# Kernel tuning notes

Measured on AMD Instinct MI355X. Metric: run time of the kernel, lower is better.

Reference implementation:

```python
import jax, jax.numpy as jnp
import numpy as np

N_NODES = 100000
N_EDGES = 1600000
IN_FEAT, HIDDEN, N_CLASSES = 512, 32, 16


def setup_inputs() -> dict:
    key = jax.random.key(0)
    k1, k2, k3, k4 = jax.random.split(key, 4)
    x = jax.random.normal(k1, (N_NODES, IN_FEAT), dtype=jnp.float32)
    edge_index = jax.random.randint(k2, (2, N_EDGES), 0, N_NODES, dtype=jnp.int64)
    W1 = jax.random.normal(k3, (IN_FEAT, HIDDEN), dtype=jnp.float32) * (1.0 / np.sqrt(IN_FEAT))
    b1 = jnp.zeros((HIDDEN,), dtype=jnp.float32)
    W2 = jax.random.normal(k4, (HIDDEN, N_CLASSES), dtype=jnp.float32) * (1.0 / np.sqrt(HIDDEN))
    b2 = jnp.zeros((N_CLASSES,), dtype=jnp.float32)
    return {"x": x, "edge_index": edge_index, "W1": W1, "b1": b1, "W2": W2, "b2": b2}


def gcn_conv(x, row, col, norm, W, b, n_nodes):
    # linear transform first (PyG GCNConv order), then gather-scale-scatter
    h = x @ W                                   # [N, F_out]
    msg = h[row] * norm[:, None]                # edge-gather + normalize
    out = jax.ops.segment_sum(msg, col, num_segments=n_nodes)
    return out + b


def gcn_norm(edge_index, n_nodes):
    # add self-loops, symmetric normalization deg^{-1/2}[row]*deg^{-1/2}[col]
    loop = jnp.arange(n_nodes, dtype=edge_index.dtype)
    row = jnp.concatenate([edge_index[0], loop])
    col = jnp.concatenate([edge_index[1], loop])
    deg = jax.ops.segment_sum(jnp.ones_like(col, dtype=jnp.float32), col, num_segments=n_nodes)
    dis = jnp.where(deg > 0, jax.lax.rsqrt(jnp.maximum(deg, 1.0)), 0.0)
    norm = dis[row] * dis[col]
    return row, col, norm


def reference(x, edge_index, W1, b1, W2, b2):
    n_nodes = x.shape[0]
    row, col, norm = gcn_norm(edge_index, n_nodes)
    h = gcn_conv(x, row, col, norm, W1, b1, n_nodes)
    h = jax.nn.relu(h)
    # dropout p=0.5 in eval mode -> identity (deterministic baseline)
    h = gcn_conv(h, row, col, norm, W2, b2, n_nodes)
    return jax.nn.log_softmax(h, axis=1)
```

## Files before the change

kernel.cpp:

```cpp
#include <hip/hip_runtime.h>
#include <hip/hip_bf16.h>

#define NN 100000
#define NE 1600000
#define FIN 512
#define FH 32
#define FC 16
#define NCB2 ((NE / 8 + 255) / 256)
#define M_SL 32
#define SLICE (NE / M_SL)
#define QSL (SLICE / 4)
#define PSZ 32768
#define NP ((NN + PSZ - 1) / PSZ)
#define NHB (M_SL * NP)
#define NGB1 ((NN + 63) / 64)
#define XW (NN / 4)
#define XSB ((XW + 255) / 256)
#define SOS_NB 98
#define SCALE_B ((NN * 8 + 1023) / 1024)

typedef __attribute__((ext_vector_type(8))) short bf16x8;
typedef __attribute__((ext_vector_type(4))) float f32x4;

__device__ inline unsigned short f2bf(float f) {
    unsigned u = __float_as_uint(f);
    return (unsigned short)((u + 0x7FFFu + ((u >> 16) & 1u)) >> 16);
}
__device__ inline float bf2f(unsigned short u) {
    return __uint_as_float(((unsigned)u) << 16);
}
__device__ inline unsigned pk2bf(float a, float b) {
    __hip_bfloat162 p = __float22bfloat162_rn(make_float2(a, b));
    union { __hip_bfloat162 h; unsigned u; } c;
    c.h = p;
    return c.u;
}


__global__ __launch_bounds__(256) void k_prep(const float* __restrict__ W1,
                                              unsigned short* __restrict__ wbuf) {
    for (int idx = threadIdx.x; idx < 16 * 2 * 64; idx += 256) {
        int s = idx >> 7;
        int t = (idx >> 6) & 1;
        int l = idx & 63;
        int k0 = s * 32 + (l >> 4) * 8;
        int c = t * 16 + (l & 15);
        bf16x8 w;
#pragma unroll
        for (int i = 0; i < 8; ++i) w[i] = (short)f2bf(W1[(size_t)(k0 + i) * FH + c]);
        *(bf16x8*)(wbuf + (size_t)idx * 8) = w;
    }
}


__global__ __launch_bounds__(256) void k_hist_gemm1(const int* __restrict__ col,
                                                    unsigned char* __restrict__ ghist,
                                                    unsigned char* __restrict__ rank,
                                                    const float* __restrict__ x,
                                                    const unsigned short* __restrict__ wbuf,
                                                    unsigned* __restrict__ h1p) {
    __shared__ int sh[PSZ / 4];

    if (blockIdx.x >= NGB1) {
        int hb = blockIdx.x - NGB1;
        int p = hb / M_SL;
        int m = hb % M_SL;
        int base = p * PSZ;
        int nb = min(PSZ, NN - base);
        int nw = (nb + 3) >> 2;
        unsigned* shw = (unsigned*)sh;
        for (int i = threadIdx.x; i < nw; i += 256) shw[i] = 0u;
        __syncthreads();
        const int4* c4p = (const int4*)(col + m * SLICE);
        for (int it = 0; it < (QSL + 255) / 256; ++it) {
            int q = it * 256 + threadIdx.x;
            if (q < QSL) {
                int4 c4 = c4p[q];
                int e = m * SLICE + q * 4;
                int cc[4] = {c4.x, c4.y, c4.z, c4.w};
#pragma unroll
                for (int u = 0; u < 4; ++u) {
                    int d = cc[u] - base;
                    if ((unsigned)d < (unsigned)nb) {
                        int sft = 8 * (d & 3);
                        unsigned old = atomicAdd(&shw[d >> 2], 1u << sft);
                        rank[e + u] = (unsigned char)((old >> sft) & 0xFFu);
                    }
                }
            }
        }
        __syncthreads();
        unsigned* gdst = (unsigned*)(ghist + (size_t)m * NN + base);
        for (int i = threadIdx.x; i < nw; i += 256) gdst[i] = shw[i];
        return;
    }

    unsigned short* lb = (unsigned short*)sh;
    for (int i = threadIdx.x; i < 2048; i += 256)
        ((int4*)lb)[i] = ((const int4*)wbuf)[i];
    __syncthreads();

    int wave = threadIdx.x >> 6;
    int lane = threadIdx.x & 63;
    int rowbase = blockIdx.x * 64 + wave * 16;
    int arow = rowbase + (lane & 15);
    int arowc = min(arow, NN - 1);
    int kgrp = (lane >> 4) * 8;

    f32x4 acc0 = {0.f, 0.f, 0.f, 0.f};
    f32x4 acc1 = {0.f, 0.f, 0.f, 0.f};
    const float* xrow = x + (size_t)arowc * FIN + kgrp;

    for (int sg = 0; sg < 16; sg += 4) {
        float4 av[8];
#pragma unroll
        for (int u = 0; u < 4; ++u) {
            av[2 * u]     = *(const float4*)(xrow + (sg + u) * 32);
            av[2 * u + 1] = *(const float4*)(xrow + (sg + u) * 32 + 4);
        }
#pragma unroll
        for (int u = 0; u < 4; ++u) {
            const float* s0 = (const float*)&av[2 * u];
            const float* s1 = (const float*)&av[2 * u + 1];
            union { bf16x8 v; unsigned w[4]; } af;
            af.w[0] = pk2bf(s0[0], s0[1]);
            af.w[1] = pk2bf(s0[2], s0[3]);
            af.w[2] = pk2bf(s1[0], s1[1]);
            af.w[3] = pk2bf(s1[2], s1[3]);
            int s = sg + u;
            bf16x8 b0 = *(const bf16x8*)(lb + ((size_t)(s * 2 + 0) * 64 + lane) * 8);
            bf16x8 b1 = *(const bf16x8*)(lb + ((size_t)(s * 2 + 1) * 64 + lane) * 8);
            acc0 = __builtin_amdgcn_mfma_f32_16x16x32_bf16(af.v, b0, acc0, 0, 0, 0);
            acc1 = __builtin_amdgcn_mfma_f32_16x16x32_bf16(af.v, b1, acc1, 0, 0, 0);
        }
    }

    int crow = rowbase + (lane >> 4) * 4;
    int ccol = lane & 15;
#pragma unroll
    for (int r = 0; r < 4; ++r) {
        if (crow + r < NN)
            h1p[(size_t)(crow + r) * 16 + ccol] = pk2bf(acc0[r], acc1[r]);
    }
}


__global__ __launch_bounds__(256) void k_xscan(unsigned* __restrict__ ghistw,
                                               int* __restrict__ cnt,
                                               float* __restrict__ dis,
                                               int* __restrict__ part) {
    __shared__ int red[256];
    int widx = blockIdx.x * 256 + threadIdx.x;
    int tot = 0;
    if (widx < XW) {
        unsigned s0 = 0, s1 = 0, s2 = 0, s3 = 0;
        unsigned* p = ghistw + widx;
#pragma unroll 4
        for (int m = 0; m < M_SL; ++m) {
            unsigned w = p[(size_t)m * XW];
            p[(size_t)m * XW] = s0 | (s1 << 8) | (s2 << 16) | (s3 << 24);
            s0 += w & 0xFFu; s1 += (w >> 8) & 0xFFu;
            s2 += (w >> 16) & 0xFFu; s3 += (w >> 24) & 0xFFu;
        }
        int c0 = widx * 4;
        *(int4*)(cnt + c0) = make_int4(s0, s1, s2, s3);
        *(float4*)(dis + c0) = make_float4(rsqrtf((float)s0 + 1.f), rsqrtf((float)s1 + 1.f),
                                           rsqrtf((float)s2 + 1.f), rsqrtf((float)s3 + 1.f));
        tot = s0 + s1 + s2 + s3;
    }
    red[threadIdx.x] = tot;
    __syncthreads();
    for (int st = 128; st > 0; st >>= 1) {
        if (threadIdx.x < st) red[threadIdx.x] += red[threadIdx.x + st];
        __syncthreads();
    }
    if (threadIdx.x == 0) part[blockIdx.x] = red[0];
}


__global__ __launch_bounds__(1024) void k_scan_off_scale(const int* __restrict__ cnt,
                                                         const int* __restrict__ part,
                                                         int* __restrict__ off,
                                                         const uint2* __restrict__ h1p2,
                                                         uint2* __restrict__ h1s2,
                                                         const float* __restrict__ dis) {
    int bid = blockIdx.x;
    if (bid < SOS_NB) {
        __shared__ int s[1024];
        __shared__ int sp[128];
        if (threadIdx.x < 128) sp[threadIdx.x] = (threadIdx.x < XSB) ? part[threadIdx.x] : 0;
        __syncthreads();
        for (int st = 1; st < 128; st <<= 1) {
            int a = (threadIdx.x < 128 && threadIdx.x >= st) ? sp[threadIdx.x - st] : 0;
            __syncthreads();
            if (threadIdx.x < 128) sp[threadIdx.x] += a;
            __syncthreads();
        }
        int pbase = (bid == 0) ? 0 : sp[bid - 1];
        int i = bid * 1024 + threadIdx.x;
        int v = (i < NN) ? cnt[i] : 0;
        s[threadIdx.x] = v;
        __syncthreads();
        for (int st = 1; st < 1024; st <<= 1) {
            int a = (threadIdx.x >= st) ? s[threadIdx.x - st] : 0;
            __syncthreads();
            s[threadIdx.x] += a;
            __syncthreads();
        }
        if (i < NN) off[i] = pbase + s[threadIdx.x] - v;
        if (i == NN - 1) off[NN] = pbase + s[threadIdx.x];
    } else {
        int idx = (bid - SOS_NB) * 1024 + threadIdx.x;
        if (idx < NN * 8) {
            uint2 v = h1p2[idx];
            float d = dis[idx >> 3];
            float a0 = bf2f((unsigned short)v.x), a1 = bf2f((unsigned short)(v.x >> 16));
            float a2 = bf2f((unsigned short)v.y), a3 = bf2f((unsigned short)(v.y >> 16));
            uint2 o;
            o.x = pk2bf(a0 * d, a1 * d);
            o.y = pk2bf(a2 * d, a3 * d);
            h1s2[idx] = o;
        }
    }
}


__global__ void k_fill(const int* __restrict__ row, const int* __restrict__ col,
                       const unsigned char* __restrict__ rank,
                       const int* __restrict__ off,
                       const unsigned char* __restrict__ ghist,
                       int* __restrict__ esrc) {
    int t = blockIdx.x * blockDim.x + threadIdx.x;
    if (t >= NE / 8) return;
#pragma unroll
    for (int qq = 0; qq < 2; ++qq) {
        int i = t * 2 + qq;
        int m = i / QSL;
        int4 r4 = ((const int4*)row)[i];
        int4 c4 = ((const int4*)col)[i];
        uchar4 rk4 = ((const uchar4*)rank)[i];
        int rr[4] = {r4.x, r4.y, r4.z, r4.w};
        int cc[4] = {c4.x, c4.y, c4.z, c4.w};
        int rk[4] = {rk4.x, rk4.y, rk4.z, rk4.w};
        int o4[4], bp[4];
#pragma unroll
        for (int u = 0; u < 4; ++u) o4[u] = off[cc[u]];
#pragma unroll
        for (int u = 0; u < 4; ++u) bp[u] = ghist[(size_t)m * NN + cc[u]];
#pragma unroll
        for (int u = 0; u < 4; ++u) esrc[o4[u] + bp[u] + rk[u]] = rr[u];
    }
}


__global__ __launch_bounds__(256) void k_gather1g2(const int* __restrict__ off,
                                                   const int* __restrict__ esrc,
                                                   const unsigned* __restrict__ h1s,
                                                   const float* __restrict__ dis,
                                                   const float* __restrict__ b1,
                                                   const float* __restrict__ W2,
                                                   float* __restrict__ h2s) {
    __shared__ float w2l[FH * FC];
    __shared__ float hrl[32][FH + 2];
    for (int i = threadIdx.x; i < FH * FC; i += 256) w2l[i] = W2[i];

    int ng = threadIdx.x >> 3;
    int l = threadIdx.x & 7;
    int g = blockIdx.x * 32 + ng;
    int s0 = off[g], s1 = off[g + 1];
    const uint2* hp = (const uint2*)h1s + l;
    float a00 = 0.f, a01 = 0.f, a02 = 0.f, a03 = 0.f;
    float a10 = 0.f, a11 = 0.f, a12 = 0.f, a13 = 0.f;
    float a20 = 0.f, a21 = 0.f, a22 = 0.f, a23 = 0.f;
    float a30 = 0.f, a31 = 0.f, a32 = 0.f, a33 = 0.f;
    int i = s0;
    for (; i + 3 < s1; i += 4) {
        int r0 = esrc[i], r1 = esrc[i + 1], r2 = esrc[i + 2], r3 = esrc[i + 3];
        uint2 w0 = hp[(size_t)r0 * 8];
        uint2 w1 = hp[(size_t)r1 * 8];
        uint2 w2 = hp[(size_t)r2 * 8];
        uint2 w3 = hp[(size_t)r3 * 8];
        a00 += bf2f((unsigned short)w0.x); a01 += bf2f((unsigned short)(w0.x >> 16));
        a02 += bf2f((unsigned short)w0.y); a03 += bf2f((unsigned short)(w0.y >> 16));
        a10 += bf2f((unsigned short)w1.x); a11 += bf2f((unsigned short)(w1.x >> 16));
        a12 += bf2f((unsigned short)w1.y); a13 += bf2f((unsigned short)(w1.y >> 16));
        a20 += bf2f((unsigned short)w2.x); a21 += bf2f((unsigned short)(w2.x >> 16));
        a22 += bf2f((unsigned short)w2.y); a23 += bf2f((unsigned short)(w2.y >> 16));
        a30 += bf2f((unsigned short)w3.x); a31 += bf2f((unsigned short)(w3.x >> 16));
        a32 += bf2f((unsigned short)w3.y); a33 += bf2f((unsigned short)(w3.y >> 16));
    }
    for (; i < s1; ++i) {
        uint2 w = hp[(size_t)esrc[i] * 8];
        a00 += bf2f((unsigned short)w.x); a01 += bf2f((unsigned short)(w.x >> 16));
        a02 += bf2f((unsigned short)w.y); a03 += bf2f((unsigned short)(w.y >> 16));
    }
    uint2 ws = hp[(size_t)g * 8];
    float f0 = a00 + a10 + a20 + a30 + bf2f((unsigned short)ws.x);
    float f16 = a01 + a11 + a21 + a31 + bf2f((unsigned short)(ws.x >> 16));
    float f1 = a02 + a12 + a22 + a32 + bf2f((unsigned short)ws.y);
    float f17 = a03 + a13 + a23 + a33 + bf2f((unsigned short)(ws.y >> 16));
    float dg = dis[g];
    float2 blo = ((const float2*)b1)[l];
    float2 bhi = ((const float2*)b1)[l + 8];
    float v0 = dg * f0 + blo.x;
    float v1 = dg * f1 + blo.y;
    float v16 = dg * f16 + bhi.x;
    float v17 = dg * f17 + bhi.y;
    *(float2*)&hrl[ng][2 * l] = make_float2(v0 > 0.f ? v0 : 0.f, v1 > 0.f ? v1 : 0.f);
    *(float2*)&hrl[ng][2 * l + 16] = make_float2(v16 > 0.f ? v16 : 0.f, v17 > 0.f ? v17 : 0.f);
    __syncthreads();

    int j = threadIdx.x & 15;
#pragma unroll
    for (int half = 0; half < 2; ++half) {
        int n2 = (threadIdx.x >> 4) + half * 16;
        int g2 = blockIdx.x * 32 + n2;
        float s = 0.0f;
#pragma unroll
        for (int k = 0; k < FH; ++k) s += hrl[n2][k] * w2l[k * FC + j];
        h2s[(size_t)g2 * FC + j] = s * dis[g2];
    }
}


__global__ __launch_bounds__(256) void k_gather2(const int* __restrict__ off,
                                                 const int* __restrict__ esrc,
                                                 const float* __restrict__ h2s,
                                                 const float* __restrict__ dis,
                                                 const float* __restrict__ b2,
                                                 float* __restrict__ out) {
    int ng = threadIdx.x >> 2;
    int l = threadIdx.x & 3;
    int g = blockIdx.x * 64 + ng;
    if (g >= NN) return;
    int s0 = off[g], s1 = off[g + 1];
    const float4* hp = (const float4*)h2s + l;
    float ax0 = 0.f, ay0 = 0.f, az0 = 0.f, aw0 = 0.f;
    float ax1 = 0.f, ay1 = 0.f, az1 = 0.f, aw1 = 0.f;
    float ax2 = 0.f, ay2 = 0.f, az2 = 0.f, aw2 = 0.f;
    float ax3 = 0.f, ay3 = 0.f, az3 = 0.f, aw3 = 0.f;
    int i = s0;
    for (; i + 3 < s1; i += 4) {
        int r0 = esrc[i], r1 = esrc[i + 1], r2 = esrc[i + 2], r3 = esrc[i + 3];
        float4 t0 = hp[(size_t)r0 * 4];
        float4 t1 = hp[(size_t)r1 * 4];
        float4 t2 = hp[(size_t)r2 * 4];
        float4 t3 = hp[(size_t)r3 * 4];
        ax0 += t0.x; ay0 += t0.y; az0 += t0.z; aw0 += t0.w;
        ax1 += t1.x; ay1 += t1.y; az1 += t1.z; aw1 += t1.w;
        ax2 += t2.x; ay2 += t2.y; az2 += t2.z; aw2 += t2.w;
        ax3 += t3.x; ay3 += t3.y; az3 += t3.z; aw3 += t3.w;
    }
    for (; i < s1; ++i) {
        float4 t = hp[(size_t)esrc[i] * 4];
        ax0 += t.x; ay0 += t.y; az0 += t.z; aw0 += t.w;
    }
    float4 ts = hp[(size_t)g * 4];
    float vx = ax0 + ax1 + ax2 + ax3 + ts.x;
    float vy = ay0 + ay1 + ay2 + ay3 + ts.y;
    float vz = az0 + az1 + az2 + az3 + ts.z;
    float vw = aw0 + aw1 + aw2 + aw3 + ts.w;
    float dg = dis[g];
    float4 bb = ((const float4*)b2)[l];
    vx = dg * vx + bb.x;
    vy = dg * vy + bb.y;
    vz = dg * vz + bb.z;
    vw = dg * vw + bb.w;
    float m = fmaxf(fmaxf(vx, vy), fmaxf(vz, vw));
#pragma unroll
    for (int o = 1; o < 4; o <<= 1) m = fmaxf(m, __shfl_xor(m, o, 4));
    float e = __expf(vx - m) + __expf(vy - m) + __expf(vz - m) + __expf(vw - m);
    float s = e;
#pragma unroll
    for (int o = 1; o < 4; o <<= 1) s += __shfl_xor(s, o, 4);
    float ls = m + logf(s);
    ((float4*)out)[(size_t)g * 4 + l] = make_float4(vx - ls, vy - ls, vz - ls, vw - ls);
}

extern "C" void kernel_launch(void* const* d_in, const int* in_sizes, int n_in,
                              void* d_out, int out_size, void* d_ws, size_t ws_size,
                              hipStream_t stream) {
    const float* x  = (const float*)d_in[0];
    const int*   ei = (const int*)d_in[1];
    const float* W1 = (const float*)d_in[2];
    const float* b1 = (const float*)d_in[3];
    const float* W2 = (const float*)d_in[4];
    const float* b2 = (const float*)d_in[5];
    float* out = (float*)d_out;

    const int* row = ei;
    const int* col = ei + NE;

    int* base = (int*)d_ws;
    unsigned char* ghist = (unsigned char*)base;
    unsigned char* rank  = ghist + (size_t)M_SL * NN;
    int*   cnt   = base + 800000 + 400000;
    int*   off   = cnt + NN;
    int*   part  = off + NN + 8;
    float* dis   = (float*)(part + 128);
    unsigned short* wbuf = (unsigned short*)(dis + NN);
    unsigned* h1p = (unsigned*)(wbuf + 16384);
    unsigned* h1s = h1p + (size_t)NN * 16;
    int*   esrc  = (int*)(h1s + (size_t)NN * 16);
    float* h2s   = (float*)h1p;

    const int B = 256;

    k_prep<<<1, B, 0, stream>>>(W1, wbuf);
    k_hist_gemm1<<<NGB1 + NHB, B, 0, stream>>>(col, ghist, rank, x, wbuf, h1p);
    k_xscan<<<XSB, B, 0, stream>>>((unsigned*)ghist, cnt, dis, part);
    k_scan_off_scale<<<SOS_NB + SCALE_B, 1024, 0, stream>>>(cnt, part, off,
                                                            (const uint2*)h1p, (uint2*)h1s, dis);
    k_fill<<<NCB2, B, 0, stream>>>(row, col, rank, off, ghist, esrc);
    k_gather1g2<<<NN / 32, B, 0, stream>>>(off, esrc, h1s, dis, b1, W2, h2s);
    k_gather2<<<(NN + 63) / 64, B, 0, stream>>>(off, esrc, h2s, dis, b2, out);
}
```

Measured before the change: 168.1 us.

## Precompute per-slice bucket bases and widen gather1 to 16-byte row loads

The scan kernel now writes a combined per-slice base array (offset plus slice histogram) so the fill kernel does one random int load per edge instead of two random loads (off and ghist). Separately, the first gather kernel now uses 4 lanes per node with uint4 (8 bf16) loads and 64 nodes per block instead of 8 lanes with uint2 loads, halving the number of scattered load instructions per edge. This costs an extra 32*NN int array written in the scan kernel and more accumulator registers in gather1.

```diff
diff --git a/kernel.cpp b/kernel.cpp
--- a/kernel.cpp
+++ b/kernel.cpp
@@ -181,6 +181,8 @@
 __global__ __launch_bounds__(1024) void k_scan_off_scale(const int* __restrict__ cnt,
                                                          const int* __restrict__ part,
                                                          int* __restrict__ off,
+                                                         const unsigned char* __restrict__ ghist,
+                                                         int* __restrict__ cb,
                                                          const uint2* __restrict__ h1p2,
                                                          uint2* __restrict__ h1s2,
                                                          const float* __restrict__ dis) {
@@ -207,7 +209,13 @@
             s[threadIdx.x] += a;
             __syncthreads();
         }
-        if (i < NN) off[i] = pbase + s[threadIdx.x] - v;
+        if (i < NN) {
+            int o = pbase + s[threadIdx.x] - v;
+            off[i] = o;
+#pragma unroll 4
+            for (int m = 0; m < M_SL; ++m)
+                cb[(size_t)m * NN + i] = o + (int)ghist[(size_t)m * NN + i];
+        }
         if (i == NN - 1) off[NN] = pbase + s[threadIdx.x];
     } else {
         int idx = (bid - SOS_NB) * 1024 + threadIdx.x;
@@ -227,8 +235,7 @@
 
 __global__ void k_fill(const int* __restrict__ row, const int* __restrict__ col,
                        const unsigned char* __restrict__ rank,
-                       const int* __restrict__ off,
-                       const unsigned char* __restrict__ ghist,
+                       const int* __restrict__ cb,
                        int* __restrict__ esrc) {
     int t = blockIdx.x * blockDim.x + threadIdx.x;
     if (t >= NE / 8) return;
@@ -242,83 +249,106 @@
         int rr[4] = {r4.x, r4.y, r4.z, r4.w};
         int cc[4] = {c4.x, c4.y, c4.z, c4.w};
         int rk[4] = {rk4.x, rk4.y, rk4.z, rk4.w};
-        int o4[4], bp[4];
-#pragma unroll
-        for (int u = 0; u < 4; ++u) o4[u] = off[cc[u]];
-#pragma unroll
-        for (int u = 0; u < 4; ++u) bp[u] = ghist[(size_t)m * NN + cc[u]];
-#pragma unroll
-        for (int u = 0; u < 4; ++u) esrc[o4[u] + bp[u] + rk[u]] = rr[u];
+        int b4[4];
+#pragma unroll
+        for (int u = 0; u < 4; ++u) b4[u] = cb[(size_t)m * NN + cc[u]];
+#pragma unroll
+        for (int u = 0; u < 4; ++u) esrc[b4[u] + rk[u]] = rr[u];
     }
 }
 
 
 __global__ __launch_bounds__(256) void k_gather1g2(const int* __restrict__ off,
                                                    const int* __restrict__ esrc,
-                                                   const unsigned* __restrict__ h1s,
+                                                   const uint4* __restrict__ h1s4,
                                                    const float* __restrict__ dis,
                                                    const float* __restrict__ b1,
                                                    const float* __restrict__ W2,
                                                    float* __restrict__ h2s) {
     __shared__ float w2l[FH * FC];
-    __shared__ float hrl[32][FH + 2];
+    __shared__ float hrl[64][FH + 4];
     for (int i = threadIdx.x; i < FH * FC; i += 256) w2l[i] = W2[i];
 
-    int ng = threadIdx.x >> 3;
-    int l = threadIdx.x & 7;
-    int g = blockIdx.x * 32 + ng;
-    int s0 = off[g], s1 = off[g + 1];
-    const uint2* hp = (const uint2*)h1s + l;
-    float a00 = 0.f, a01 = 0.f, a02 = 0.f, a03 = 0.f;
-    float a10 = 0.f, a11 = 0.f, a12 = 0.f, a13 = 0.f;
-    float a20 = 0.f, a21 = 0.f, a22 = 0.f, a23 = 0.f;
-    float a30 = 0.f, a31 = 0.f, a32 = 0.f, a33 = 0.f;
-    int i = s0;
-    for (; i + 3 < s1; i += 4) {
-        int r0 = esrc[i], r1 = esrc[i + 1], r2 = esrc[i + 2], r3 = esrc[i + 3];
-        uint2 w0 = hp[(size_t)r0 * 8];
-        uint2 w1 = hp[(size_t)r1 * 8];
-        uint2 w2 = hp[(size_t)r2 * 8];
-        uint2 w3 = hp[(size_t)r3 * 8];
-        a00 += bf2f((unsigned short)w0.x); a01 += bf2f((unsigned short)(w0.x >> 16));
-        a02 += bf2f((unsigned short)w0.y); a03 += bf2f((unsigned short)(w0.y >> 16));
-        a10 += bf2f((unsigned short)w1.x); a11 += bf2f((unsigned short)(w1.x >> 16));
-        a12 += bf2f((unsigned short)w1.y); a13 += bf2f((unsigned short)(w1.y >> 16));
-        a20 += bf2f((unsigned short)w2.x); a21 += bf2f((unsigned short)(w2.x >> 16));
-        a22 += bf2f((unsigned short)w2.y); a23 += bf2f((unsigned short)(w2.y >> 16));
-        a30 += bf2f((unsigned short)w3.x); a31 += bf2f((unsigned short)(w3.x >> 16));
-        a32 += bf2f((unsigned short)w3.y); a33 += bf2f((unsigned short)(w3.y >> 16));
-    }
-    for (; i < s1; ++i) {
-        uint2 w = hp[(size_t)esrc[i] * 8];
-        a00 += bf2f((unsigned short)w.x); a01 += bf2f((unsigned short)(w.x >> 16));
-        a02 += bf2f((unsigned short)w.y); a03 += bf2f((unsigned short)(w.y >> 16));
-    }
-    uint2 ws = hp[(size_t)g * 8];
-    float f0 = a00 + a10 + a20 + a30 + bf2f((unsigned short)ws.x);
-    float f16 = a01 + a11 + a21 + a31 + bf2f((unsigned short)(ws.x >> 16));
-    float f1 = a02 + a12 + a22 + a32 + bf2f((unsigned short)ws.y);
-    float f17 = a03 + a13 + a23 + a33 + bf2f((unsigned short)(ws.y >> 16));
-    float dg = dis[g];
-    float2 blo = ((const float2*)b1)[l];
-    float2 bhi = ((const float2*)b1)[l + 8];
-    float v0 = dg * f0 + blo.x;
-    float v1 = dg * f1 + blo.y;
-    float v16 = dg * f16 + bhi.x;
-    float v17 = dg * f17 + bhi.y;
-    *(float2*)&hrl[ng][2 * l] = make_float2(v0 > 0.f ? v0 : 0.f, v1 > 0.f ? v1 : 0.f);
-    *(float2*)&hrl[ng][2 * l + 16] = make_float2(v16 > 0.f ? v16 : 0.f, v17 > 0.f ? v17 : 0.f);
+    int ng = threadIdx.x >> 2;
+    int l = threadIdx.x & 3;
+    int g = blockIdx.x * 64 + ng;
+    if (g < NN) {
+        int s0 = off[g], s1 = off[g + 1];
+        const uint4* hp = h1s4 + l;
+        float acc[4][8];
+#pragma unroll
+        for (int u = 0; u < 4; ++u)
+#pragma unroll
+            for (int k = 0; k < 8; ++k) acc[u][k] = 0.f;
+        int i = s0;
+        for (; i + 3 < s1; i += 4) {
+            int r0 = esrc[i], r1 = esrc[i + 1], r2 = esrc[i + 2], r3 = esrc[i + 3];
+            uint4 w0 = hp[(size_t)r0 * 4];
+            uint4 w1 = hp[(size_t)r1 * 4];
+            uint4 w2 = hp[(size_t)r2 * 4];
+            uint4 w3 = hp[(size_t)r3 * 4];
+            acc[0][0] += bf2f((unsigned short)w0.x); acc[0][1] += bf2f((unsigned short)(w0.x >> 16));
+            acc[0][2] += bf2f((unsigned short)w0.y); acc[0][3] += bf2f((unsigned short)(w0.y >> 16));
+            acc[0][4] += bf2f((unsigned short)w0.z); acc[0][5] += bf2f((unsigned short)(w0.z >> 16));
+            acc[0][6] += bf2f((unsigned short)w0.w); acc[0][7] += bf2f((unsigned short)(w0.w >> 16));
+            acc[1][0] += bf2f((unsigned short)w1.x); acc[1][1] += bf2f((unsigned short)(w1.x >> 16));
+            acc[1][2] += bf2f((unsigned short)w1.y); acc[1][3] += bf2f((unsigned short)(w1.y >> 16));
+            acc[1][4] += bf2f((unsigned short)w1.z); acc[1][5] += bf2f((unsigned short)(w1.z >> 16));
+            acc[1][6] += bf2f((unsigned short)w1.w); acc[1][7] += bf2f((unsigned short)(w1.w >> 16));
+            acc[2][0] += bf2f((unsigned short)w2.x); acc[2][1] += bf2f((unsigned short)(w2.x >> 16));
+            acc[2][2] += bf2f((unsigned short)w2.y); acc[2][3] += bf2f((unsigned short)(w2.y >> 16));
+            acc[2][4] += bf2f((unsigned short)w2.z); acc[2][5] += bf2f((unsigned short)(w2.z >> 16));
+            acc[2][6] += bf2f((unsigned short)w2.w); acc[2][7] += bf2f((unsigned short)(w2.w >> 16));
+            acc[3][0] += bf2f((unsigned short)w3.x); acc[3][1] += bf2f((unsigned short)(w3.x >> 16));
+            acc[3][2] += bf2f((unsigned short)w3.y); acc[3][3] += bf2f((unsigned short)(w3.y >> 16));
+            acc[3][4] += bf2f((unsigned short)w3.z); acc[3][5] += bf2f((unsigned short)(w3.z >> 16));
+            acc[3][6] += bf2f((unsigned short)w3.w); acc[3][7] += bf2f((unsigned short)(w3.w >> 16));
+        }
+        for (; i < s1; ++i) {
+            uint4 w = hp[(size_t)esrc[i] * 4];
+            acc[0][0] += bf2f((unsigned short)w.x); acc[0][1] += bf2f((unsigned short)(w.x >> 16));
+            acc[0][2] += bf2f((unsigned short)w.y); acc[0][3] += bf2f((unsigned short)(w.y >> 16));
+            acc[0][4] += bf2f((unsigned short)w.z); acc[0][5] += bf2f((unsigned short)(w.z >> 16));
+            acc[0][6] += bf2f((unsigned short)w.w); acc[0][7] += bf2f((unsigned short)(w.w >> 16));
+        }
+        uint4 ws = hp[(size_t)g * 4];
+        acc[0][0] += bf2f((unsigned short)ws.x); acc[0][1] += bf2f((unsigned short)(ws.x >> 16));
+        acc[0][2] += bf2f((unsigned short)ws.y); acc[0][3] += bf2f((unsigned short)(ws.y >> 16));
+        acc[0][4] += bf2f((unsigned short)ws.z); acc[0][5] += bf2f((unsigned short)(ws.z >> 16));
+        acc[0][6] += bf2f((unsigned short)ws.w); acc[0][7] += bf2f((unsigned short)(ws.w >> 16));
+        float dg = dis[g];
+        float4 blo = ((const float4*)b1)[l];
+        float4 bhi = ((const float4*)b1)[l + 4];
+        float f0 = acc[0][0] + acc[1][0] + acc[2][0] + acc[3][0];
+        float f1 = acc[0][2] + acc[1][2] + acc[2][2] + acc[3][2];
+        float f2 = acc[0][4] + acc[1][4] + acc[2][4] + acc[3][4];
+        float f3 = acc[0][6] + acc[1][6] + acc[2][6] + acc[3][6];
+        float h0 = acc[0][1] + acc[1][1] + acc[2][1] + acc[3][1];
+        float h1 = acc[0][3] + acc[1][3] + acc[2][3] + acc[3][3];
+        float h2 = acc[0][5] + acc[1][5] + acc[2][5] + acc[3][5];
+        float h3 = acc[0][7] + acc[1][7] + acc[2][7] + acc[3][7];
+        float v0 = dg * f0 + blo.x, v1 = dg * f1 + blo.y;
+        float v2 = dg * f2 + blo.z, v3 = dg * f3 + blo.w;
+        float u0 = dg * h0 + bhi.x, u1 = dg * h1 + bhi.y;
+        float u2 = dg * h2 + bhi.z, u3 = dg * h3 + bhi.w;
+        *(float4*)&hrl[ng][4 * l] = make_float4(v0 > 0.f ? v0 : 0.f, v1 > 0.f ? v1 : 0.f,
+                                                v2 > 0.f ? v2 : 0.f, v3 > 0.f ? v3 : 0.f);
+        *(float4*)&hrl[ng][4 * l + 16] = make_float4(u0 > 0.f ? u0 : 0.f, u1 > 0.f ? u1 : 0.f,
+                                                     u2 > 0.f ? u2 : 0.f, u3 > 0.f ? u3 : 0.f);
+    }
     __syncthreads();
 
     int j = threadIdx.x & 15;
 #pragma unroll
-    for (int half = 0; half < 2; ++half) {
-        int n2 = (threadIdx.x >> 4) + half * 16;
-        int g2 = blockIdx.x * 32 + n2;
-        float s = 0.0f;
-#pragma unroll
-        for (int k = 0; k < FH; ++k) s += hrl[n2][k] * w2l[k * FC + j];
-        h2s[(size_t)g2 * FC + j] = s * dis[g2];
+    for (int q = 0; q < 4; ++q) {
+        int n2 = (threadIdx.x >> 4) + q * 16;
+        int g2 = blockIdx.x * 64 + n2;
+        if (g2 < NN) {
+            float s = 0.0f;
+#pragma unroll
+            for (int k = 0; k < FH; ++k) s += hrl[n2][k] * w2l[k * FC + j];
+            h2s[(size_t)g2 * FC + j] = s * dis[g2];
+        }
     }
 }
 
@@ -402,6 +432,7 @@
     unsigned* h1p = (unsigned*)(wbuf + 16384);
     unsigned* h1s = h1p + (size_t)NN * 16;
     int*   esrc  = (int*)(h1s + (size_t)NN * 16);
+    int*   cb    = esrc + NE;
     float* h2s   = (float*)h1p;
 
     const int B = 256;
@@ -409,9 +440,9 @@
     k_prep<<<1, B, 0, stream>>>(W1, wbuf);
     k_hist_gemm1<<<NGB1 + NHB, B, 0, stream>>>(col, ghist, rank, x, wbuf, h1p);
     k_xscan<<<XSB, B, 0, stream>>>((unsigned*)ghist, cnt, dis, part);
-    k_scan_off_scale<<<SOS_NB + SCALE_B, 1024, 0, stream>>>(cnt, part, off,
+    k_scan_off_scale<<<SOS_NB + SCALE_B, 1024, 0, stream>>>(cnt, part, off, ghist, cb,
                                                             (const uint2*)h1p, (uint2*)h1s, dis);
-    k_fill<<<NCB2, B, 0, stream>>>(row, col, rank, off, ghist, esrc);
-    k_gather1g2<<<NN / 32, B, 0, stream>>>(off, esrc, h1s, dis, b1, W2, h2s);
+    k_fill<<<NCB2, B, 0, stream>>>(row, col, rank, cb, esrc);
+    k_gather1g2<<<(NN + 63) / 64, B, 0, stream>>>(off, esrc, (const uint4*)h1s, dis, b1, W2, h2s);
     k_gather2<<<(NN + 63) / 64, B, 0, stream>>>(off, esrc, h2s, dis, b2, out);
 }
```

Result: slower. 184.0 us (+9.4%).
